# Kernel tuning notes

Measured on AMD Instinct MI355X. Metric: run time of the kernel, lower is better.

## Reference

```python
import jax, jax.numpy as jnp
import numpy as np

EPS = 1e-8  # torch.cosine_similarity default eps


def setup_inputs() -> dict:
    key = jax.random.key(0)
    k1, k2 = jax.random.split(key)
    B, S, C, W = 8, 75, 64, 19
    support_x = jax.random.normal(k1, (B, S, C, W, W), dtype=jnp.float32)
    query_x = jax.random.normal(k2, (B, S, C, W, W), dtype=jnp.float32)
    return {"support_x": support_x, "query_x": query_x}


def reference(support_x, query_x):
    # support_x, query_x: [B, S, C, W, W]
    # For each support spatial location (i,j), cosine-similarity of its C-vector
    # against every query spatial location (p,q), then max over (p,q).
    B, S, C, W, _ = support_x.shape
    s_norm = jnp.linalg.norm(support_x, axis=2)  # [B,S,W,W]
    q_norm = jnp.linalg.norm(query_x, axis=2)    # [B,S,W,W]
    # Pairwise dot products over channels: [B,S,Wi,Wj,Wp,Wq]
    num = jnp.einsum('bscij,bscpq->bsijpq', support_x, query_x)
    denom = jnp.maximum(s_norm[:, :, :, :, None, None] * q_norm[:, :, None, None, :, :], EPS)
    sim = num / denom
    out = jnp.max(sim, axis=(-2, -1))  # max over query spatial grid -> [B,S,W,W]
    # loop order was i (rows) then j (cols), concatenated on last dim == row-major reshape
    return out.reshape(B, S, W * W)
```

## Files before the change

### kernel.cpp

```cpp
#include <hip/hip_runtime.h>
#include <hip/hip_bf16.h>
#include <stdint.h>

#define WW   361
#define CCH  64
#define MH   192
#define NP   368
#define NBS  600
#define NTHR 768

typedef __attribute__((ext_vector_type(8))) short short8;
typedef __attribute__((ext_vector_type(4))) float f32x4;


__device__ __forceinline__ float stage_row(const float* __restrict__ gp,
                                           unsigned short* __restrict__ dst, int sw) {
  float a0 = 0.f, a1 = 0.f, a2 = 0.f, a3 = 0.f;
  #pragma unroll
  for (int c = 0; c < 8; ++c) {
    float v[8];
    #pragma unroll
    for (int j = 0; j < 8; ++j) v[j] = gp[(c * 8 + j) * WW];
    unsigned int u[4];
    #pragma unroll
    for (int jj = 0; jj < 4; ++jj) {
      a0 += v[2*jj] * v[2*jj];
      a1 += v[2*jj+1] * v[2*jj+1];
      __hip_bfloat162 b2 =
          __float22bfloat162_rn(make_float2(v[2*jj], v[2*jj+1]));
      u[jj] = *(unsigned int*)&b2;
    }
    *(uint4*)&dst[(c ^ sw) * 8] = make_uint4(u[0], u[1], u[2], u[3]);
  }
  return rsqrtf((a0 + a1) + (a2 + a3));
}

__device__ __forceinline__ void zero_row(unsigned short* __restrict__ dst) {
  #pragma unroll
  for (int c = 0; c < 8; ++c)
    *(uint4*)&dst[c * 8] = make_uint4(0u, 0u, 0u, 0u);
}

__global__ __launch_bounds__(NTHR, 6) void cossim_max_kernel(
    const float* __restrict__ support, const float* __restrict__ query,
    float* __restrict__ out)
{
  __shared__ __align__(16) unsigned short S_sh[MH * CCH];
  __shared__ __align__(16) unsigned short Q_sh[NP * CCH];
  __shared__ float inv_s[MH];
  __shared__ float inv_q[NP];

  const int tid   = threadIdx.x;
  const int bs    = blockIdx.x >> 1;
  const int half  = blockIdx.x & 1;
  const int mBase = half * MH;

  const float* sg = support + (size_t)bs * (WW * CCH);
  const float* qg = query   + (size_t)bs * (WW * CCH);

  if (tid < NP) {
    const int m = tid;
    if (m < WW) {
      inv_q[m] = stage_row(qg + m, &Q_sh[m * CCH], m & 7);
    } else {
      zero_row(&Q_sh[m * CCH]);
      inv_q[m] = 0.f;
    }
  } else if (tid < NP + MH) {
    const int mL = tid - NP;
    const int mG = mBase + mL;
    if (mG < WW) {
      inv_s[mL] = stage_row(sg + mG, &S_sh[mL * CCH], mL & 7);
    } else {
      zero_row(&S_sh[mL * CCH]);
      inv_s[mL] = 0.f;
    }
  }
  __syncthreads();

  const int lane = tid & 63;
  const int wv   = tid >> 6;
  const int l15  = lane & 15;
  const int quad = lane >> 4;

  short8 af[2];
  {
    const int m = 16 * wv + l15;
    #pragma unroll
    for (int s = 0; s < 2; ++s) {
      const int c = 4 * s + quad;
      af[s] = *(const short8*)&S_sh[m * CCH + ((c ^ (m & 7)) * 8)];
    }
  }

  f32x4 mx = {-3e38f, -3e38f, -3e38f, -3e38f};

  for (int pt = 0; pt < NP / 16; ++pt) {
    const int n  = 16 * pt + l15;
    const int sw = l15 & 7;
    short8 b0 = *(const short8*)&Q_sh[n * CCH + (((0 + quad) ^ sw) * 8)];
    short8 b1 = *(const short8*)&Q_sh[n * CCH + (((4 + quad) ^ sw) * 8)];
    f32x4 acc = {0.f, 0.f, 0.f, 0.f};
    acc = __builtin_amdgcn_mfma_f32_16x16x32_bf16(af[0], b0, acc, 0, 0, 0);
    acc = __builtin_amdgcn_mfma_f32_16x16x32_bf16(af[1], b1, acc, 0, 0, 0);
    const float qs   = inv_q[n];
    const float bias = (n < WW) ? 0.f : -1e30f;
    #pragma unroll
    for (int r = 0; r < 4; ++r) mx[r] = fmaxf(mx[r], acc[r] * qs + bias);
  }

  #pragma unroll
  for (int d = 1; d < 16; d <<= 1) {
    #pragma unroll
    for (int r = 0; r < 4; ++r) mx[r] = fmaxf(mx[r], __shfl_xor(mx[r], d));
  }

  if (l15 == 0) {
    #pragma unroll
    for (int r = 0; r < 4; ++r) {
      const int mL = 16 * wv + 4 * quad + r;
      const int iG = mBase + mL;
      if (iG < WW) out[(size_t)bs * WW + iG] = mx[r] * inv_s[mL];
    }
  }
}

extern "C" void kernel_launch(void* const* d_in, const int* in_sizes, int n_in,
                              void* d_out, int out_size, void* d_ws, size_t ws_size,
                              hipStream_t stream) {
  const float* support = (const float*)d_in[0];
  const float* query   = (const float*)d_in[1];
  float* out = (float*)d_out;
  dim3 grid(NBS * 2), block(NTHR);
  hipLaunchKernelGGL(cossim_max_kernel, grid, block, 0, stream,
                     support, query, out);
}
```

Measured before the change: 136.3 us.

## Make kernel persistent with double-buffered LDS staging overlapped with MFMA loop

Replaces the one-block-per-job grid with a persistent grid of 256 blocks that loop over 1200 jobs. The fp32 loads, bf16 conversion and norm computation for the next job are interleaved into the MFMA loop of the current job, using double-buffered LDS. The aim is to hide global load latency behind compute and to avoid per-block staging stalls. In exchange LDS use doubles, occupancy drops to 3 blocks per CU, and only 256 blocks run, which may leave some CUs underused and make the work imbalanced.

```diff
diff --git a/kernel.cpp b/kernel.cpp
--- a/kernel.cpp
+++ b/kernel.cpp
@@ -2,79 +2,87 @@
 #include <hip/hip_bf16.h>
 #include <stdint.h>
 
-#define WW   361
-#define CCH  64
-#define MH   192
-#define NP   368
-#define NBS  600
-#define NTHR 768
+#define WW    361
+#define CCH   64
+#define MH    192
+#define NP    368
+#define NT    23
+#define NJOBS 1200
+#define NTHR  768
+#define GRID  256
 
 typedef __attribute__((ext_vector_type(8))) short short8;
 typedef __attribute__((ext_vector_type(4))) float f32x4;
 
 
-__device__ __forceinline__ float stage_row(const float* __restrict__ gp,
-                                           unsigned short* __restrict__ dst, int sw) {
-  float a0 = 0.f, a1 = 0.f, a2 = 0.f, a3 = 0.f;
-  #pragma unroll
-  for (int c = 0; c < 8; ++c) {
-    float v[8];
-    #pragma unroll
-    for (int j = 0; j < 8; ++j) v[j] = gp[(c * 8 + j) * WW];
-    unsigned int u[4];
-    #pragma unroll
-    for (int jj = 0; jj < 4; ++jj) {
-      a0 += v[2*jj] * v[2*jj];
-      a1 += v[2*jj+1] * v[2*jj+1];
-      __hip_bfloat162 b2 =
-          __float22bfloat162_rn(make_float2(v[2*jj], v[2*jj+1]));
-      u[jj] = *(unsigned int*)&b2;
-    }
-    *(uint4*)&dst[(c ^ sw) * 8] = make_uint4(u[0], u[1], u[2], u[3]);
-  }
-  return rsqrtf((a0 + a1) + (a2 + a3));
-}
-
-__device__ __forceinline__ void zero_row(unsigned short* __restrict__ dst) {
-  #pragma unroll
-  for (int c = 0; c < 8; ++c)
-    *(uint4*)&dst[c * 8] = make_uint4(0u, 0u, 0u, 0u);
-}
-
-__global__ __launch_bounds__(NTHR, 6) void cossim_max_kernel(
+__global__ __launch_bounds__(NTHR, 3) void cossim_max_kernel(
     const float* __restrict__ support, const float* __restrict__ query,
     float* __restrict__ out)
 {
-  __shared__ __align__(16) unsigned short S_sh[MH * CCH];
-  __shared__ __align__(16) unsigned short Q_sh[NP * CCH];
-  __shared__ float inv_s[MH];
-  __shared__ float inv_q[NP];
+  __shared__ __align__(16) unsigned short S_sh[2][MH * CCH];
+  __shared__ __align__(16) unsigned short Q_sh[2][NP * CCH];
+  __shared__ float inv_s[2][MH];
+  __shared__ float inv_q[2][NP];
 
   const int tid   = threadIdx.x;
-  const int bs    = blockIdx.x >> 1;
-  const int half  = blockIdx.x & 1;
+  const int b     = blockIdx.x;
+  const int half  = b & 1;
   const int mBase = half * MH;
 
-  const float* sg = support + (size_t)bs * (WW * CCH);
-  const float* qg = query   + (size_t)bs * (WW * CCH);
-
-  if (tid < NP) {
-    const int m = tid;
-    if (m < WW) {
-      inv_q[m] = stage_row(qg + m, &Q_sh[m * CCH], m & 7);
-    } else {
-      zero_row(&Q_sh[m * CCH]);
-      inv_q[m] = 0.f;
-    }
-  } else if (tid < NP + MH) {
-    const int mL = tid - NP;
-    const int mG = mBase + mL;
-    if (mG < WW) {
-      inv_s[mL] = stage_row(sg + mG, &S_sh[mL * CCH], mL & 7);
-    } else {
-      zero_row(&S_sh[mL * CCH]);
-      inv_s[mL] = 0.f;
-    }
+  const bool isQ = (tid < NP);
+  const bool isS = (tid >= NP) && (tid < NP + MH);
+  const int  mRow = isQ ? tid : (tid - NP);
+  const int  gRow = isQ ? tid : (mBase + (tid - NP));
+  const bool active_row = (isQ || isS) && (gRow < WW);
+  const bool pad_row    = (isQ || isS) && !active_row;
+  const int  rsw = mRow & 7;
+
+  unsigned short* dRowA = &Q_sh[0][0];
+  unsigned short* dRowB = &Q_sh[1][0];
+  float* dInvA = &inv_q[0][0];
+  float* dInvB = &inv_q[1][0];
+  if (isQ)      { dRowA = &Q_sh[0][mRow*CCH]; dRowB = &Q_sh[1][mRow*CCH];
+                  dInvA = &inv_q[0][mRow];    dInvB = &inv_q[1][mRow]; }
+  else if (isS) { dRowA = &S_sh[0][mRow*CCH]; dRowB = &S_sh[1][mRow*CCH];
+                  dInvA = &inv_s[0][mRow];    dInvB = &inv_s[1][mRow]; }
+
+  const size_t bs0 = (size_t)(b >> 1);
+  const size_t jobstride = (size_t)128 * WW * CCH;
+  const float* g = (isQ ? query : support) + bs0 * (size_t)(WW * CCH) + gRow;
+
+  if (active_row) {
+    float v[4][8];
+    float ss = 0.f;
+    #pragma unroll
+    for (int c = 0; c < 4; ++c)
+      #pragma unroll
+      for (int j = 0; j < 8; ++j) v[c][j] = g[(c*8 + j) * WW];
+    #pragma unroll
+    for (int c = 0; c < 8; ++c) {
+      unsigned int u[4];
+      float a0 = 0.f, a1 = 0.f;
+      #pragma unroll
+      for (int jj = 0; jj < 4; ++jj) {
+        float x = v[c & 3][2*jj], y = v[c & 3][2*jj + 1];
+        a0 += x * x; a1 += y * y;
+        __hip_bfloat162 b2 = __float22bfloat162_rn(make_float2(x, y));
+        u[jj] = *(unsigned int*)&b2;
+      }
+      ss += a0 + a1;
+      *(uint4*)&dRowA[((c ^ rsw) * 8)] = make_uint4(u[0], u[1], u[2], u[3]);
+      if (c < 4) {
+        #pragma unroll
+        for (int j = 0; j < 8; ++j) v[c][j] = g[((c + 4)*8 + j) * WW];
+      }
+    }
+    dInvA[0] = rsqrtf(ss);
+  } else if (pad_row) {
+    #pragma unroll
+    for (int c = 0; c < 8; ++c) {
+      *(uint4*)&dRowA[c * 8] = make_uint4(0u, 0u, 0u, 0u);
+      *(uint4*)&dRowB[c * 8] = make_uint4(0u, 0u, 0u, 0u);
+    }
+    dInvA[0] = 0.f; dInvB[0] = 0.f;
   }
   __syncthreads();
 
@@ -82,46 +90,108 @@
   const int wv   = tid >> 6;
   const int l15  = lane & 15;
   const int quad = lane >> 4;
-
-  short8 af[2];
-  {
-    const int m = 16 * wv + l15;
-    #pragma unroll
-    for (int s = 0; s < 2; ++s) {
-      const int c = 4 * s + quad;
-      af[s] = *(const short8*)&S_sh[m * CCH + ((c ^ (m & 7)) * 8)];
-    }
-  }
-
-  f32x4 mx = {-3e38f, -3e38f, -3e38f, -3e38f};
-
-  for (int pt = 0; pt < NP / 16; ++pt) {
-    const int n  = 16 * pt + l15;
-    const int sw = l15 & 7;
-    short8 b0 = *(const short8*)&Q_sh[n * CCH + (((0 + quad) ^ sw) * 8)];
-    short8 b1 = *(const short8*)&Q_sh[n * CCH + (((4 + quad) ^ sw) * 8)];
-    f32x4 acc = {0.f, 0.f, 0.f, 0.f};
-    acc = __builtin_amdgcn_mfma_f32_16x16x32_bf16(af[0], b0, acc, 0, 0, 0);
-    acc = __builtin_amdgcn_mfma_f32_16x16x32_bf16(af[1], b1, acc, 0, 0, 0);
-    const float qs   = inv_q[n];
-    const float bias = (n < WW) ? 0.f : -1e30f;
-    #pragma unroll
-    for (int r = 0; r < 4; ++r) mx[r] = fmaxf(mx[r], acc[r] * qs + bias);
-  }
-
-  #pragma unroll
-  for (int d = 1; d < 16; d <<= 1) {
-    #pragma unroll
-    for (int r = 0; r < 4; ++r) mx[r] = fmaxf(mx[r], __shfl_xor(mx[r], d));
-  }
-
-  if (l15 == 0) {
-    #pragma unroll
-    for (int r = 0; r < 4; ++r) {
-      const int mL = 16 * wv + 4 * quad + r;
-      const int iG = mBase + mL;
-      if (iG < WW) out[(size_t)bs * WW + iG] = mx[r] * inv_s[mL];
-    }
+  const int bsw  = l15 & 7;
+  const float lastbias = (l15 < 9) ? 0.f : -1e30f;
+  const int am    = 16 * wv + l15;
+  const int aoff0 = am * CCH + (((0 + quad) ^ (am & 7)) * 8);
+  const int aoff1 = am * CCH + (((4 + quad) ^ (am & 7)) * 8);
+  const int boff0 = l15 * CCH + (((0 + quad) ^ bsw) * 8);
+  const int boff1 = l15 * CCH + (((4 + quad) ^ bsw) * 8);
+
+  int job = b;
+  int t = 0;
+  size_t outb = bs0 * WW;
+
+  for (;;) {
+    const int  cur = t & 1;
+    const bool have_next = (job + GRID) < NJOBS;
+    const float* gnext = g + jobstride;
+
+    const unsigned short* Sc = cur ? &S_sh[1][0] : &S_sh[0][0];
+    const unsigned short* Qc = cur ? &Q_sh[1][0] : &Q_sh[0][0];
+    const float*         iqc = cur ? &inv_q[1][0] : &inv_q[0][0];
+    unsigned short* dN = cur ? dRowA : dRowB;
+    float*          iN = cur ? dInvA : dInvB;
+
+    short8 af0 = *(const short8*)&Sc[aoff0];
+    short8 af1 = *(const short8*)&Sc[aoff1];
+
+    short8 bb0[2], bb1[2];
+    float  qv[2];
+    bb0[0] = *(const short8*)&Qc[boff0];
+    bb1[0] = *(const short8*)&Qc[boff1];
+    qv[0]  = iqc[l15];
+
+    f32x4 mx = {-3e38f, -3e38f, -3e38f, -3e38f};
+    float ssn = 0.f;
+    float fa[2][8];
+    const bool st = have_next && active_row;
+
+    #pragma unroll
+    for (int pt = 0; pt < NT; ++pt) {
+      const int pb = pt & 1;
+      if (pt + 1 < NT) {
+        const int nb = 16 * (pt + 1) * CCH;
+        bb0[pb ^ 1] = *(const short8*)&Qc[nb + boff0];
+        bb1[pb ^ 1] = *(const short8*)&Qc[nb + boff1];
+        qv[pb ^ 1]  = iqc[16 * (pt + 1) + l15];
+      }
+      if (st) {
+        if ((pt & 1) == 0 && pt <= 14) {
+          const int c = pt >> 1;
+          #pragma unroll
+          for (int j = 0; j < 8; ++j) fa[c & 1][j] = gnext[(c*8 + j) * WW];
+        } else if ((pt & 1) == 1 && pt >= 3 && pt <= 17) {
+          const int c = (pt - 3) >> 1;
+          unsigned int u[4];
+          float a0 = 0.f, a1 = 0.f;
+          #pragma unroll
+          for (int jj = 0; jj < 4; ++jj) {
+            float x = fa[c & 1][2*jj], y = fa[c & 1][2*jj + 1];
+            a0 += x * x; a1 += y * y;
+            __hip_bfloat162 b2 = __float22bfloat162_rn(make_float2(x, y));
+            u[jj] = *(unsigned int*)&b2;
+          }
+          ssn += a0 + a1;
+          *(uint4*)&dN[((c ^ rsw) * 8)] = make_uint4(u[0], u[1], u[2], u[3]);
+        } else if (pt == 19) {
+          iN[0] = rsqrtf(ssn);
+        }
+      }
+      f32x4 acc = {0.f, 0.f, 0.f, 0.f};
+      acc = __builtin_amdgcn_mfma_f32_16x16x32_bf16(af0, bb0[pb], acc, 0, 0, 0);
+      acc = __builtin_amdgcn_mfma_f32_16x16x32_bf16(af1, bb1[pb], acc, 0, 0, 0);
+      const float qs = qv[pb];
+      if (pt < NT - 1) {
+        #pragma unroll
+        for (int r = 0; r < 4; ++r) mx[r] = fmaxf(mx[r], acc[r] * qs);
+      } else {
+        #pragma unroll
+        for (int r = 0; r < 4; ++r) mx[r] = fmaxf(mx[r], acc[r] * qs + lastbias);
+      }
+    }
+
+    #pragma unroll
+    for (int d = 1; d < 16; d <<= 1) {
+      #pragma unroll
+      for (int r = 0; r < 4; ++r) mx[r] = fmaxf(mx[r], __shfl_xor(mx[r], d));
+    }
+    if (l15 == 0) {
+      const float* isc = cur ? &inv_s[1][0] : &inv_s[0][0];
+      #pragma unroll
+      for (int r = 0; r < 4; ++r) {
+        const int mL = 16 * wv + 4 * quad + r;
+        const int iG = mBase + mL;
+        if (iG < WW) out[outb + iG] = mx[r] * isc[mL];
+      }
+    }
+
+    if (!have_next) break;
+    __syncthreads();
+    g = gnext;
+    job += GRID;
+    ++t;
+    outb += (size_t)128 * WW;
   }
 }
 
@@ -131,7 +201,7 @@
   const float* support = (const float*)d_in[0];
   const float* query   = (const float*)d_in[1];
   float* out = (float*)d_out;
-  dim3 grid(NBS * 2), block(NTHR);
+  dim3 grid(GRID), block(NTHR);
   hipLaunchKernelGGL(cossim_max_kernel, grid, block, 0, stream,
                      support, query, out);
 }
```

Measured after the change: 140.2 us. 1.03x slower.

## Persistent blocks with atomic job queue and triple-buffered query staging

Applied to the files above, without the earlier changes.

Replaces the one-block-per-job launch with 512 persistent blocks that take (batch, half) jobs from an atomic counter. The query tile is split into four 96-row chunks that rotate through a triple-buffered LDS ring, so global loads for the next chunk and the next job's support rows overlap MFMA compute on the current chunk. Staging now spreads each row over 8 threads with a shuffle reduction for the norm, instead of one thread per row. This hides load latency and launch tail cost, in exchange for more barriers, an atomic per job, a memset before launch, and more complex control flow.

```diff
diff --git a/kernel.cpp b/kernel.cpp
--- a/kernel.cpp
+++ b/kernel.cpp
@@ -2,126 +2,210 @@
 #include <hip/hip_bf16.h>
 #include <stdint.h>
 
-#define WW   361
-#define CCH  64
-#define MH   192
-#define NP   368
-#define NBS  600
-#define NTHR 768
+#define WW    361
+#define CCH   64
+#define MH    192
+#define QC    96
+#define NPQ   384
+#define NJOBS 1200
+#define NTHR  768
+#define GRID  512
+#define WWC   (WW*CCH)
 
 typedef __attribute__((ext_vector_type(8))) short short8;
+typedef __attribute__((ext_vector_type(8))) float f32x8;
 typedef __attribute__((ext_vector_type(4))) float f32x4;
 
 
-__device__ __forceinline__ float stage_row(const float* __restrict__ gp,
-                                           unsigned short* __restrict__ dst, int sw) {
-  float a0 = 0.f, a1 = 0.f, a2 = 0.f, a3 = 0.f;
+__device__ __forceinline__ void stage_issue(f32x8& f, const float* __restrict__ base,
+                                            int row, bool v, int c8) {
+  if (v) {
+    const float* p = base + row + c8 * 8 * WW;
+    #pragma unroll
+    for (int j = 0; j < 8; ++j) f[j] = p[j * WW];
+  } else {
+    #pragma unroll
+    for (int j = 0; j < 8; ++j) f[j] = 0.f;
+  }
+}
+
+__device__ __forceinline__ void stage_write(const f32x8& f, unsigned short* __restrict__ rowdst,
+                                            float* __restrict__ invdst, bool vrow,
+                                            int lr, int c8) {
+  unsigned int u[4];
+  float a0 = 0.f, a1 = 0.f;
   #pragma unroll
-  for (int c = 0; c < 8; ++c) {
-    float v[8];
-    #pragma unroll
-    for (int j = 0; j < 8; ++j) v[j] = gp[(c * 8 + j) * WW];
-    unsigned int u[4];
-    #pragma unroll
-    for (int jj = 0; jj < 4; ++jj) {
-      a0 += v[2*jj] * v[2*jj];
-      a1 += v[2*jj+1] * v[2*jj+1];
-      __hip_bfloat162 b2 =
-          __float22bfloat162_rn(make_float2(v[2*jj], v[2*jj+1]));
-      u[jj] = *(unsigned int*)&b2;
-    }
-    *(uint4*)&dst[(c ^ sw) * 8] = make_uint4(u[0], u[1], u[2], u[3]);
-  }
-  return rsqrtf((a0 + a1) + (a2 + a3));
-}
-
-__device__ __forceinline__ void zero_row(unsigned short* __restrict__ dst) {
+  for (int jj = 0; jj < 4; ++jj) {
+    float x = f[2*jj], y = f[2*jj + 1];
+    a0 += x * x; a1 += y * y;
+    __hip_bfloat162 b2 = __float22bfloat162_rn(make_float2(x, y));
+    u[jj] = *(unsigned int*)&b2;
+  }
+  float ss = a0 + a1;
+  ss += __shfl_xor(ss, 1);
+  ss += __shfl_xor(ss, 2);
+  ss += __shfl_xor(ss, 4);
+  *(uint4*)&rowdst[((c8 ^ (lr & 7)) * 8)] = make_uint4(u[0], u[1], u[2], u[3]);
+  if (c8 == 0) invdst[0] = vrow ? rsqrtf(ss) : 0.f;
+}
+
+__device__ __forceinline__ void chunk_compute(const unsigned short* __restrict__ Qb,
+                                              const float* __restrict__ iqb,
+                                              short8 af0, short8 af1,
+                                              int boff0, int boff1, int l15,
+                                              f32x4& mx, float b4, float b5) {
   #pragma unroll
-  for (int c = 0; c < 8; ++c)
-    *(uint4*)&dst[c * 8] = make_uint4(0u, 0u, 0u, 0u);
+  for (int ptL = 0; ptL < 6; ++ptL) {
+    const int nb = ptL * 16 * CCH;
+    short8 b0 = *(const short8*)&Qb[nb + boff0];
+    short8 b1 = *(const short8*)&Qb[nb + boff1];
+    const float qs = iqb[ptL * 16 + l15];
+    f32x4 acc = {0.f, 0.f, 0.f, 0.f};
+    acc = __builtin_amdgcn_mfma_f32_16x16x32_bf16(af0, b0, acc, 0, 0, 0);
+    acc = __builtin_amdgcn_mfma_f32_16x16x32_bf16(af1, b1, acc, 0, 0, 0);
+    const float bb = (ptL == 4) ? b4 : ((ptL == 5) ? b5 : 0.f);
+    #pragma unroll
+    for (int r = 0; r < 4; ++r) mx[r] = fmaxf(mx[r], acc[r] * qs + bb);
+  }
 }
 
 __global__ __launch_bounds__(NTHR, 6) void cossim_max_kernel(
     const float* __restrict__ support, const float* __restrict__ query,
-    float* __restrict__ out)
+    float* __restrict__ out, unsigned int* __restrict__ ctr)
 {
   __shared__ __align__(16) unsigned short S_sh[MH * CCH];
-  __shared__ __align__(16) unsigned short Q_sh[NP * CCH];
+  __shared__ __align__(16) unsigned short Q_sh[3][QC * CCH];
   __shared__ float inv_s[MH];
-  __shared__ float inv_q[NP];
-
-  const int tid   = threadIdx.x;
-  const int bs    = blockIdx.x >> 1;
-  const int half  = blockIdx.x & 1;
-  const int mBase = half * MH;
-
-  const float* sg = support + (size_t)bs * (WW * CCH);
-  const float* qg = query   + (size_t)bs * (WW * CCH);
-
-  if (tid < NP) {
-    const int m = tid;
-    if (m < WW) {
-      inv_q[m] = stage_row(qg + m, &Q_sh[m * CCH], m & 7);
-    } else {
-      zero_row(&Q_sh[m * CCH]);
-      inv_q[m] = 0.f;
-    }
-  } else if (tid < NP + MH) {
-    const int mL = tid - NP;
-    const int mG = mBase + mL;
-    if (mG < WW) {
-      inv_s[mL] = stage_row(sg + mG, &S_sh[mL * CCH], mL & 7);
-    } else {
-      zero_row(&S_sh[mL * CCH]);
-      inv_s[mL] = 0.f;
-    }
-  }
-  __syncthreads();
-
+  __shared__ float inv_q[3][QC];
+  __shared__ int jslot;
+
+  const int tid  = threadIdx.x;
+  const int r    = tid >> 3;
+  const int c8   = tid & 7;
   const int lane = tid & 63;
   const int wv   = tid >> 6;
   const int l15  = lane & 15;
   const int quad = lane >> 4;
-
-  short8 af[2];
+  const int bsw  = l15 & 7;
+  const float lastbias4 = (l15 < 9) ? 0.f : -1e30f;
+
+  const int am    = 16 * wv + l15;
+  const int aoff0 = am * CCH + (((0 + quad) ^ (am & 7)) * 8);
+  const int aoff1 = am * CCH + (((4 + quad) ^ (am & 7)) * 8);
+  const int boff0 = l15 * CCH + (((0 + quad) ^ bsw) * 8);
+  const int boff1 = l15 * CCH + (((4 + quad) ^ bsw) * 8);
+
+  int j  = blockIdx.x;
+  int bs = j >> 1;
+  int mBase = (j & 1) * MH;
+  const float* qbase = query   + (size_t)bs * WWC;
+  const float* sbase = support + (size_t)bs * WWC;
+
   {
-    const int m = 16 * wv + l15;
-    #pragma unroll
-    for (int s = 0; s < 2; ++s) {
-      const int c = 4 * s + quad;
-      af[s] = *(const short8*)&S_sh[m * CCH + ((c ^ (m & 7)) * 8)];
-    }
-  }
-
-  f32x4 mx = {-3e38f, -3e38f, -3e38f, -3e38f};
-
-  for (int pt = 0; pt < NP / 16; ++pt) {
-    const int n  = 16 * pt + l15;
-    const int sw = l15 & 7;
-    short8 b0 = *(const short8*)&Q_sh[n * CCH + (((0 + quad) ^ sw) * 8)];
-    short8 b1 = *(const short8*)&Q_sh[n * CCH + (((4 + quad) ^ sw) * 8)];
-    f32x4 acc = {0.f, 0.f, 0.f, 0.f};
-    acc = __builtin_amdgcn_mfma_f32_16x16x32_bf16(af[0], b0, acc, 0, 0, 0);
-    acc = __builtin_amdgcn_mfma_f32_16x16x32_bf16(af[1], b1, acc, 0, 0, 0);
-    const float qs   = inv_q[n];
-    const float bias = (n < WW) ? 0.f : -1e30f;
-    #pragma unroll
-    for (int r = 0; r < 4; ++r) mx[r] = fmaxf(mx[r], acc[r] * qs + bias);
-  }
-
-  #pragma unroll
-  for (int d = 1; d < 16; d <<= 1) {
-    #pragma unroll
-    for (int r = 0; r < 4; ++r) mx[r] = fmaxf(mx[r], __shfl_xor(mx[r], d));
-  }
-
-  if (l15 == 0) {
-    #pragma unroll
-    for (int r = 0; r < 4; ++r) {
-      const int mL = 16 * wv + 4 * quad + r;
-      const int iG = mBase + mL;
-      if (iG < WW) out[(size_t)bs * WW + iG] = mx[r] * inv_s[mL];
-    }
+    f32x8 s0, s1, q0;
+    stage_issue(s0, sbase, mBase + r,      (mBase + r) < WW,      c8);
+    stage_issue(s1, sbase, mBase + 96 + r, (mBase + 96 + r) < WW, c8);
+    stage_issue(q0, qbase, r,              true,                  c8);
+    stage_write(s0, &S_sh[r * CCH],        &inv_s[r],      (mBase + r) < WW,      r, c8);
+    stage_write(s1, &S_sh[(96 + r) * CCH], &inv_s[96 + r], (mBase + 96 + r) < WW, r, c8);
+    stage_write(q0, &Q_sh[0][r * CCH],     &inv_q[0][r],   true,                  r, c8);
+    __syncthreads();
+  }
+
+  short8 af0 = *(const short8*)&S_sh[aoff0];
+  short8 af1 = *(const short8*)&S_sh[aoff1];
+  float  invA = inv_s[am];
+  f32x4  mx = {-3e38f, -3e38f, -3e38f, -3e38f};
+
+  f32x8 qfA, qfB, sf;
+  stage_issue(qfA, qbase, QC + r, true, c8);
+  int ib = 0;
+
+  int jn = 0; bool vn = false;
+  int mBase_n = 0;
+  const float* qbase_n = query;
+  const float* sbase_n = support;
+
+  for (;;) {
+    if (tid == 0) jslot = (int)(GRID + atomicAdd(ctr, 1u));
+    stage_issue(qfB, qbase, 2 * QC + r, true, c8);
+    chunk_compute(&Q_sh[ib][0], &inv_q[ib][0], af0, af1, boff0, boff1, l15, mx, 0.f, 0.f);
+    {
+      int ibw = ib + 1; if (ibw == 3) ibw = 0;
+      stage_write(qfA, &Q_sh[ibw][r * CCH], &inv_q[ibw][r], true, r, c8);
+    }
+    __syncthreads();
+    {
+      int js = jslot;
+      jn = __builtin_amdgcn_readfirstlane(js);
+      vn = (jn < NJOBS);
+      int bsn = vn ? (jn >> 1) : 0;
+      mBase_n = (jn & 1) * MH;
+      qbase_n = query   + (size_t)bsn * WWC;
+      sbase_n = support + (size_t)bsn * WWC;
+    }
+    ib = (ib + 1 == 3) ? 0 : ib + 1;
+
+    stage_issue(qfA, qbase, 3 * QC + r, (3 * QC + r) < WW, c8);
+    if (vn) stage_issue(sf, sbase_n, mBase_n + r, (mBase_n + r) < WW, c8);
+    chunk_compute(&Q_sh[ib][0], &inv_q[ib][0], af0, af1, boff0, boff1, l15, mx, 0.f, 0.f);
+    {
+      int ibw = ib + 1; if (ibw == 3) ibw = 0;
+      stage_write(qfB, &Q_sh[ibw][r * CCH], &inv_q[ibw][r], true, r, c8);
+    }
+    __syncthreads();
+    ib = (ib + 1 == 3) ? 0 : ib + 1;
+
+    if (vn) stage_issue(qfB, qbase_n, r, true, c8);
+    chunk_compute(&Q_sh[ib][0], &inv_q[ib][0], af0, af1, boff0, boff1, l15, mx, 0.f, 0.f);
+    {
+      int ibw = ib + 1; if (ibw == 3) ibw = 0;
+      stage_write(qfA, &Q_sh[ibw][r * CCH], &inv_q[ibw][r], (3 * QC + r) < WW, r, c8);
+    }
+    if (vn) {
+      stage_write(sf, &S_sh[r * CCH], &inv_s[r], (mBase_n + r) < WW, r, c8);
+      stage_issue(sf, sbase_n, mBase_n + 96 + r, (mBase_n + 96 + r) < WW, c8);
+    }
+    __syncthreads();
+    ib = (ib + 1 == 3) ? 0 : ib + 1;
+
+    if (vn) stage_issue(qfA, qbase_n, QC + r, true, c8);
+    chunk_compute(&Q_sh[ib][0], &inv_q[ib][0], af0, af1, boff0, boff1, l15, mx,
+                  lastbias4, -1e30f);
+    #pragma unroll
+    for (int d = 1; d < 16; d <<= 1) {
+      #pragma unroll
+      for (int rr = 0; rr < 4; ++rr) mx[rr] = fmaxf(mx[rr], __shfl_xor(mx[rr], d));
+    }
+    {
+      const float iv0 = __shfl(invA, 4 * quad + 0);
+      const float iv1 = __shfl(invA, 4 * quad + 1);
+      const float iv2 = __shfl(invA, 4 * quad + 2);
+      const float iv3 = __shfl(invA, 4 * quad + 3);
+      if (l15 == 0) {
+        const size_t ob = (size_t)bs * WW;
+        const int mL = 16 * wv + 4 * quad;
+        if (mBase + mL + 0 < WW) out[ob + mBase + mL + 0] = mx[0] * iv0;
+        if (mBase + mL + 1 < WW) out[ob + mBase + mL + 1] = mx[1] * iv1;
+        if (mBase + mL + 2 < WW) out[ob + mBase + mL + 2] = mx[2] * iv2;
+        if (mBase + mL + 3 < WW) out[ob + mBase + mL + 3] = mx[3] * iv3;
+      }
+    }
+    {
+      int ibw = ib + 1; if (ibw == 3) ibw = 0;
+      if (vn) stage_write(qfB, &Q_sh[ibw][r * CCH], &inv_q[ibw][r], true, r, c8);
+    }
+    if (vn) stage_write(sf, &S_sh[(96 + r) * CCH], &inv_s[96 + r],
+                        (mBase_n + 96 + r) < WW, r, c8);
+    __syncthreads();
+    if (!vn) break;
+
+    j = jn; bs = jn >> 1; mBase = mBase_n; qbase = qbase_n; sbase = sbase_n;
+    af0 = *(const short8*)&S_sh[aoff0];
+    af1 = *(const short8*)&S_sh[aoff1];
+    invA = inv_s[am];
+    mx[0] = -3e38f; mx[1] = -3e38f; mx[2] = -3e38f; mx[3] = -3e38f;
+    ib = (ib + 1 == 3) ? 0 : ib + 1;
   }
 }
 
@@ -131,7 +215,9 @@
   const float* support = (const float*)d_in[0];
   const float* query   = (const float*)d_in[1];
   float* out = (float*)d_out;
-  dim3 grid(NBS * 2), block(NTHR);
+  unsigned int* ctr = (unsigned int*)d_ws;
+  hipMemsetAsync(ctr, 0, sizeof(unsigned int), stream);
+  dim3 grid(GRID), block(NTHR);
   hipLaunchKernelGGL(cossim_max_kernel, grid, block, 0, stream,
-                     support, query, out);
-}
+                     support, query, out, ctr);
+}
```

New measurement: 524.5 us. 3.85x slower.

## Load support fragments directly into registers and shrink block to 512 threads

Applied to the files above, without the earlier changes.

Support rows no longer go through shared memory. Each wave gathers its A fragments straight from global memory into registers, computes the norms with lane shuffles, and overlaps this gather with query staging. Blocks drop to 8 waves, and the upper four waves each handle two M tiles that reuse the same B fragments. The change also adds a block-index swizzle across XCDs, raises MFMA priority with s_setprio, and applies the padding bias only on the last tile. The aim is to cut LDS traffic and sync cost, at the price of uneven per-wave work and strided global gathers.

```diff
diff --git a/kernel.cpp b/kernel.cpp
--- a/kernel.cpp
+++ b/kernel.cpp
@@ -2,12 +2,13 @@
 #include <hip/hip_bf16.h>
 #include <stdint.h>
 
-#define WW   361
-#define CCH  64
-#define MH   192
-#define NP   368
-#define NBS  600
-#define NTHR 768
+#define WW    361
+#define CCH   64
+#define MH    192
+#define NQR   368
+#define NT    23
+#define NTHR  512
+#define WWC   (WW*CCH)
 
 typedef __attribute__((ext_vector_type(8))) short short8;
 typedef __attribute__((ext_vector_type(4))) float f32x4;
@@ -15,7 +16,7 @@
 
 __device__ __forceinline__ float stage_row(const float* __restrict__ gp,
                                            unsigned short* __restrict__ dst, int sw) {
-  float a0 = 0.f, a1 = 0.f, a2 = 0.f, a3 = 0.f;
+  float a0 = 0.f, a1 = 0.f;
   #pragma unroll
   for (int c = 0; c < 8; ++c) {
     float v[8];
@@ -26,103 +27,167 @@
     for (int jj = 0; jj < 4; ++jj) {
       a0 += v[2*jj] * v[2*jj];
       a1 += v[2*jj+1] * v[2*jj+1];
-      __hip_bfloat162 b2 =
-          __float22bfloat162_rn(make_float2(v[2*jj], v[2*jj+1]));
+      __hip_bfloat162 b2 = __float22bfloat162_rn(make_float2(v[2*jj], v[2*jj+1]));
       u[jj] = *(unsigned int*)&b2;
     }
     *(uint4*)&dst[(c ^ sw) * 8] = make_uint4(u[0], u[1], u[2], u[3]);
   }
-  return rsqrtf((a0 + a1) + (a2 + a3));
+  return rsqrtf(a0 + a1);
 }
 
 __device__ __forceinline__ void zero_row(unsigned short* __restrict__ dst) {
   #pragma unroll
   for (int c = 0; c < 8; ++c)
     *(uint4*)&dst[c * 8] = make_uint4(0u, 0u, 0u, 0u);
+}
+
+__device__ __forceinline__ void gatherA(const float* __restrict__ srow, bool valid,
+                                        int quad, f32x4& w0, f32x4& w1,
+                                        f32x4& w2, f32x4& w3) {
+  if (valid) {
+    #pragma unroll
+    for (int j = 0; j < 4; ++j) w0[j] = srow[(8 * quad + j) * WW];
+    #pragma unroll
+    for (int j = 0; j < 4; ++j) w1[j] = srow[(8 * quad + 4 + j) * WW];
+    #pragma unroll
+    for (int j = 0; j < 4; ++j) w2[j] = srow[(32 + 8 * quad + j) * WW];
+    #pragma unroll
+    for (int j = 0; j < 4; ++j) w3[j] = srow[(32 + 8 * quad + 4 + j) * WW];
+  } else {
+    w0 = (f32x4){0.f, 0.f, 0.f, 0.f}; w1 = w0; w2 = w0; w3 = w0;
+  }
+}
+
+__device__ __forceinline__ void buildA(f32x4 w0, f32x4 w1, f32x4 w2, f32x4 w3,
+                                       bool valid, short8& af0, short8& af1,
+                                       float& invA) {
+  unsigned int u[8];
+  float ss = 0.f;
+  #pragma unroll
+  for (int p = 0; p < 2; ++p) {
+    __hip_bfloat162 b2 = __float22bfloat162_rn(make_float2(w0[2*p], w0[2*p+1]));
+    u[p] = *(unsigned int*)&b2;
+    ss += w0[2*p] * w0[2*p] + w0[2*p+1] * w0[2*p+1];
+    b2 = __float22bfloat162_rn(make_float2(w1[2*p], w1[2*p+1]));
+    u[2 + p] = *(unsigned int*)&b2;
+    ss += w1[2*p] * w1[2*p] + w1[2*p+1] * w1[2*p+1];
+    b2 = __float22bfloat162_rn(make_float2(w2[2*p], w2[2*p+1]));
+    u[4 + p] = *(unsigned int*)&b2;
+    ss += w2[2*p] * w2[2*p] + w2[2*p+1] * w2[2*p+1];
+    b2 = __float22bfloat162_rn(make_float2(w3[2*p], w3[2*p+1]));
+    u[6 + p] = *(unsigned int*)&b2;
+    ss += w3[2*p] * w3[2*p] + w3[2*p+1] * w3[2*p+1];
+  }
+  ss += __shfl_xor(ss, 16);
+  ss += __shfl_xor(ss, 32);
+  uint4 t0 = make_uint4(u[0], u[1], u[2], u[3]);
+  uint4 t1 = make_uint4(u[4], u[5], u[6], u[7]);
+  af0 = *(short8*)&t0;
+  af1 = *(short8*)&t1;
+  invA = valid ? rsqrtf(ss) : 0.f;
+}
+
+__device__ __forceinline__ void epilogue(f32x4 mx, float invA, int tileBase,
+                                         int quad, int l15,
+                                         float* __restrict__ outb) {
+  #pragma unroll
+  for (int d = 1; d < 16; d <<= 1) {
+    #pragma unroll
+    for (int r = 0; r < 4; ++r) mx[r] = fmaxf(mx[r], __shfl_xor(mx[r], d));
+  }
+  const float iv0 = __shfl(invA, 4 * quad + 0);
+  const float iv1 = __shfl(invA, 4 * quad + 1);
+  const float iv2 = __shfl(invA, 4 * quad + 2);
+  const float iv3 = __shfl(invA, 4 * quad + 3);
+  if (l15 == 0) {
+    const int mb = tileBase + 4 * quad;
+    if (mb + 0 < WW) outb[mb + 0] = mx[0] * iv0;
+    if (mb + 1 < WW) outb[mb + 1] = mx[1] * iv1;
+    if (mb + 2 < WW) outb[mb + 2] = mx[2] * iv2;
+    if (mb + 3 < WW) outb[mb + 3] = mx[3] * iv3;
+  }
 }
 
 __global__ __launch_bounds__(NTHR, 6) void cossim_max_kernel(
     const float* __restrict__ support, const float* __restrict__ query,
     float* __restrict__ out)
 {
-  __shared__ __align__(16) unsigned short S_sh[MH * CCH];
-  __shared__ __align__(16) unsigned short Q_sh[NP * CCH];
-  __shared__ float inv_s[MH];
-  __shared__ float inv_q[NP];
-
-  const int tid   = threadIdx.x;
-  const int bs    = blockIdx.x >> 1;
-  const int half  = blockIdx.x & 1;
-  const int mBase = half * MH;
-
-  const float* sg = support + (size_t)bs * (WW * CCH);
-  const float* qg = query   + (size_t)bs * (WW * CCH);
-
-  if (tid < NP) {
-    const int m = tid;
-    if (m < WW) {
-      inv_q[m] = stage_row(qg + m, &Q_sh[m * CCH], m & 7);
-    } else {
-      zero_row(&Q_sh[m * CCH]);
-      inv_q[m] = 0.f;
-    }
-  } else if (tid < NP + MH) {
-    const int mL = tid - NP;
-    const int mG = mBase + mL;
-    if (mG < WW) {
-      inv_s[mL] = stage_row(sg + mG, &S_sh[mL * CCH], mL & 7);
-    } else {
-      zero_row(&S_sh[mL * CCH]);
-      inv_s[mL] = 0.f;
-    }
-  }
-  __syncthreads();
+  __shared__ __align__(16) unsigned short Q_sh[NQR * CCH];
+  __shared__ float inv_q[NQR];
+
+  const int tid  = threadIdx.x;
+  const int b    = ((int)blockIdx.x & 7) * 150 + ((int)blockIdx.x >> 3);
+  const int bs   = b >> 1;
+  const int mBase = (b & 1) * MH;
 
   const int lane = tid & 63;
   const int wv   = tid >> 6;
   const int l15  = lane & 15;
   const int quad = lane >> 4;
 
-  short8 af[2];
-  {
-    const int m = 16 * wv + l15;
-    #pragma unroll
-    for (int s = 0; s < 2; ++s) {
-      const int c = 4 * s + quad;
-      af[s] = *(const short8*)&S_sh[m * CCH + ((c ^ (m & 7)) * 8)];
+  const float* sg = support + (size_t)bs * WWC;
+  const float* qg = query   + (size_t)bs * WWC;
+
+  const int t0   = wv;
+  const int t1   = wv + 4;
+  const bool two = (wv >= 4);
+  const int iG0  = mBase + 16 * t0 + l15;
+  const int iG1  = mBase + 16 * t1 + l15;
+
+  f32x4 w0, w1, w2, w3;
+  gatherA(sg + iG0, iG0 < WW, quad, w0, w1, w2, w3);
+
+  if (tid < NQR) {
+    if (tid < WW) inv_q[tid] = stage_row(qg + tid, &Q_sh[tid * CCH], tid & 7);
+    else { zero_row(&Q_sh[tid * CCH]); inv_q[tid] = 0.f; }
+  }
+
+  short8 af00, af01; float invA0;
+  buildA(w0, w1, w2, w3, iG0 < WW, af00, af01, invA0);
+
+  short8 af10 = af00, af11 = af01; float invA1 = 0.f;
+  if (two) {
+    gatherA(sg + iG1, iG1 < WW, quad, w0, w1, w2, w3);
+    buildA(w0, w1, w2, w3, iG1 < WW, af10, af11, invA1);
+  }
+
+  __syncthreads();
+
+  const int boff0 = l15 * CCH + ((quad       ^ (l15 & 7)) * 8);
+  const int boff1 = l15 * CCH + (((4 + quad) ^ (l15 & 7)) * 8);
+  const float lastbias = (l15 < 9) ? 0.f : -1e30f;
+  const bool t1live = two && (mBase + 16 * t1) < WW;
+
+  f32x4 mx0 = {-3e38f, -3e38f, -3e38f, -3e38f};
+  f32x4 mx1 = mx0;
+
+  for (int t = 0; t < NT; ++t) {
+    const int nb = t * 16 * CCH;
+    short8 b0 = *(const short8*)&Q_sh[nb + boff0];
+    short8 b1 = *(const short8*)&Q_sh[nb + boff1];
+    const float qs = inv_q[t * 16 + l15];
+    const float bb = (t == NT - 1) ? lastbias : 0.f;
+    f32x4 acc = {0.f, 0.f, 0.f, 0.f};
+    __builtin_amdgcn_s_setprio(1);
+    acc = __builtin_amdgcn_mfma_f32_16x16x32_bf16(af00, b0, acc, 0, 0, 0);
+    acc = __builtin_amdgcn_mfma_f32_16x16x32_bf16(af01, b1, acc, 0, 0, 0);
+    __builtin_amdgcn_s_setprio(0);
+    #pragma unroll
+    for (int r = 0; r < 4; ++r) mx0[r] = fmaxf(mx0[r], acc[r] * qs + bb);
+    if (t1live) {
+      f32x4 acc2 = {0.f, 0.f, 0.f, 0.f};
+      __builtin_amdgcn_s_setprio(1);
+      acc2 = __builtin_amdgcn_mfma_f32_16x16x32_bf16(af10, b0, acc2, 0, 0, 0);
+      acc2 = __builtin_amdgcn_mfma_f32_16x16x32_bf16(af11, b1, acc2, 0, 0, 0);
+      __builtin_amdgcn_s_setprio(0);
+      #pragma unroll
+      for (int r = 0; r < 4; ++r) mx1[r] = fmaxf(mx1[r], acc2[r] * qs + bb);
     }
   }
 
-  f32x4 mx = {-3e38f, -3e38f, -3e38f, -3e38f};
-
-  for (int pt = 0; pt < NP / 16; ++pt) {
-    const int n  = 16 * pt + l15;
-    const int sw = l15 & 7;
-    short8 b0 = *(const short8*)&Q_sh[n * CCH + (((0 + quad) ^ sw) * 8)];
-    short8 b1 = *(const short8*)&Q_sh[n * CCH + (((4 + quad) ^ sw) * 8)];
-    f32x4 acc = {0.f, 0.f, 0.f, 0.f};
-    acc = __builtin_amdgcn_mfma_f32_16x16x32_bf16(af[0], b0, acc, 0, 0, 0);
-    acc = __builtin_amdgcn_mfma_f32_16x16x32_bf16(af[1], b1, acc, 0, 0, 0);
-    const float qs   = inv_q[n];
-    const float bias = (n < WW) ? 0.f : -1e30f;
-    #pragma unroll
-    for (int r = 0; r < 4; ++r) mx[r] = fmaxf(mx[r], acc[r] * qs + bias);
-  }
-
-  #pragma unroll
-  for (int d = 1; d < 16; d <<= 1) {
-    #pragma unroll
-    for (int r = 0; r < 4; ++r) mx[r] = fmaxf(mx[r], __shfl_xor(mx[r], d));
-  }
-
-  if (l15 == 0) {
-    #pragma unroll
-    for (int r = 0; r < 4; ++r) {
-      const int mL = 16 * wv + 4 * quad + r;
-      const int iG = mBase + mL;
-      if (iG < WW) out[(size_t)bs * WW + iG] = mx[r] * inv_s[mL];
-    }
-  }
+  float* outb = out + (size_t)bs * WW;
+  epilogue(mx0, invA0, mBase + 16 * t0, quad, l15, outb);
+  if (t1live) epilogue(mx1, invA1, mBase + 16 * t1, quad, l15, outb);
 }
 
 extern "C" void kernel_launch(void* const* d_in, const int* in_sizes, int n_in,
@@ -131,7 +196,7 @@
   const float* support = (const float*)d_in[0];
   const float* query   = (const float*)d_in[1];
   float* out = (float*)d_out;
-  dim3 grid(NBS * 2), block(NTHR);
+  dim3 grid(1200), block(NTHR);
   hipLaunchKernelGGL(cossim_max_kernel, grid, block, 0, stream,
                      support, query, out);
 }
```

Result: slower. 201.5 us (+47.8%).
